# Optimization experiments

Measured on AMD Instinct MI355X. Metric: run time of the kernel, lower is better.

The kernel has to match this reference:

```python
import jax, jax.numpy as jnp
import numpy as np

N_HEAD = 16
ROPE_BASE = 10000.0


def _rope(x, cos, sin):
    # x: [B,H,T,D]; cos/sin: [T,D/2] broadcast over B,H
    half = x.shape[-1] // 2
    x1, x2 = x[..., :half], x[..., half:]
    return jnp.concatenate([x1 * cos - x2 * sin, x1 * sin + x2 * cos], axis=-1)


def setup_inputs() -> dict:
    key = jax.random.key(0)
    k1, k2, k3 = jax.random.split(key, 3)
    C = 2048
    x = jax.random.normal(k1, (4, 2048, C), dtype=jnp.float32)
    w_qkv = jax.random.normal(k2, (C, 3 * C), dtype=jnp.float32) * 0.02
    w_proj = jax.random.normal(k3, (C, C), dtype=jnp.float32) * 0.02
    return {"x": x, "w_qkv": w_qkv, "w_proj": w_proj}


def reference(x, w_qkv, w_proj):
    B, T, C = x.shape
    H = N_HEAD
    D = C // H
    half = D // 2

    qkv = x @ w_qkv  # [B,T,3C]
    q, k, v = jnp.split(qkv, 3, axis=-1)
    # [B,T,C] -> [B,H,T,D]
    q = q.reshape(B, T, H, D).transpose(0, 2, 1, 3)
    k = k.reshape(B, T, H, D).transpose(0, 2, 1, 3)
    v = v.reshape(B, T, H, D).transpose(0, 2, 1, 3)

    # RoPE cache (start_pos = 0, no kv_cache / prefill path)
    inv_freq = 1.0 / (ROPE_BASE ** (jnp.arange(half, dtype=jnp.float32) / half))
    pos = jnp.arange(T, dtype=jnp.float32)
    freqs = pos[:, None] * inv_freq[None, :]  # [T, half]
    cos, sin = jnp.cos(freqs), jnp.sin(freqs)

    q = _rope(q, cos, sin)
    k = _rope(k, cos, sin)

    # scaled dot-product attention with explicit causal mask
    att = jnp.einsum("bhqd,bhkd->bhqk", q, k) / jnp.sqrt(jnp.asarray(D, x.dtype))
    causal = jnp.arange(T)[:, None] >= jnp.arange(T)[None, :]  # [T,T] bool
    att = jnp.where(causal, att, jnp.asarray(-jnp.inf, att.dtype))
    att = jax.nn.softmax(att, axis=-1)
    # dropout = identity (eval mode)
    out = jnp.einsum("bhqk,bhkd->bhqd", att, v)
    out = out.transpose(0, 2, 1, 3).reshape(B, T, C)
    out = out @ w_proj
    return out, k, v  # (output, new kv-cache)
```

## Files before the change

### kernel.cpp

```cpp
#include <hip/hip_runtime.h>
#include <math.h>

#define CDIM 2048
#define TDIM 2048
#define BDIM 4
#define HDIM 16
#define DDIM 128
#define M1   (BDIM * TDIM)
#define N1   (3 * CDIM)
#define KK   CDIM
#define NT   32

typedef unsigned short u16;
typedef __bf16 bf16x8 __attribute__((ext_vector_type(8)));
typedef float f32x4 __attribute__((ext_vector_type(4)));

__device__ __forceinline__ u16 f2b(float f) {
  union { float f; unsigned u; } x; x.f = f;
  unsigned r = x.u + 0x7fffu + ((x.u >> 16) & 1u);
  return (u16)(r >> 16);
}

__device__ __forceinline__ void gload_lds16(const void* g, void* l) {
  __builtin_amdgcn_global_load_lds(
      (__attribute__((address_space(1))) void*)g,
      (__attribute__((address_space(3))) void*)l, 16, 0, 0);
}

__global__ void convert_x(const float* __restrict__ x, u16* __restrict__ xb, int n4) {
  int i = blockIdx.x * blockDim.x + threadIdx.x;
  if (i < n4) {
    float4 v = ((const float4*)x)[i];
    unsigned long long o = (unsigned long long)f2b(v.x)
                         | ((unsigned long long)f2b(v.y) << 16)
                         | ((unsigned long long)f2b(v.z) << 32)
                         | ((unsigned long long)f2b(v.w) << 48);
    ((unsigned long long*)xb)[i] = o;
  }
}

__global__ void transpose_w(const float* __restrict__ w, u16* __restrict__ wt, int K, int N) {
  __shared__ float tile[32][33];
  const int n0 = blockIdx.x * 32, k0 = blockIdx.y * 32;
  const int tx = threadIdx.x & 31, ty = threadIdx.x >> 5;
  for (int r = ty; r < 32; r += 8)
    tile[r][tx] = w[(k0 + r) * N + n0 + tx];
  __syncthreads();
  for (int r = ty; r < 32; r += 8)
    wt[(n0 + r) * K + k0 + tx] = f2b(tile[tx][r]);
}

__global__ void rope_tab(float* __restrict__ cosT, float* __restrict__ sinT) {
  int i = blockIdx.x * blockDim.x + threadIdx.x;
  int t = i >> 6, d = i & 63;
  double inv = pow(10000.0, -(double)d / 64.0);
  double a = (double)t * inv;
  cosT[i] = (float)cos(a);
  sinT[i] = (float)sin(a);
}

__global__ void transpose_v(const float* __restrict__ v, u16* __restrict__ vt) {
  __shared__ float tile[32][33];
  const int bh = blockIdx.z;
  const int t0 = blockIdx.x * 32, d0 = blockIdx.y * 32;
  const int tx = threadIdx.x & 31, ty = threadIdx.x >> 5;
  const float* src = v + (bh * TDIM + t0) * DDIM + d0;
  for (int r = ty; r < 32; r += 8)
    tile[r][tx] = src[r * DDIM + tx];
  __syncthreads();
  u16* dst = vt + (bh * DDIM + d0) * TDIM + t0;
  for (int r = ty; r < 32; r += 8)
    dst[r * TDIM + tx] = f2b(tile[tx][r]);
}


#define VMW4 asm volatile("s_waitcnt vmcnt(4)" ::: "memory");
#define VMW2 asm volatile("s_waitcnt vmcnt(2)" ::: "memory");
#define VMW0 asm volatile("s_waitcnt vmcnt(0)" ::: "memory");
#define NOWAIT

#define GEMM256_TILE(bufA_, bufB_, nA_, nB_, kno_, STG, WMID, WEND)            \
  {                                                                            \
    __builtin_amdgcn_s_barrier();        \
    bf16x8 aX[4][2], aY[4][2], bX[2][2], bY[2][2];                             \
                                                     \
    _Pragma("unroll")                                                          \
    for (int i = 0; i < 4; ++i)                                                \
      _Pragma("unroll")                                                        \
      for (int kh = 0; kh < 2; ++kh)                                           \
        aX[i][kh] = *(const bf16x8*)&(bufA_)[aoff + i * 1024 +                 \
                                             (((kh * 4 + quad) ^ rsw) * 8)];   \
    _Pragma("unroll")                                                          \
    for (int j = 0; j < 2; ++j)                                                \
      _Pragma("unroll")                                                        \
      for (int kh = 0; kh < 2; ++kh)                                           \
        bX[j][kh] = *(const bf16x8*)&(bufB_)[boff + j * 1024 +                 \
                                             (((kh * 4 + quad) ^ rsw) * 8)];   \
                                                          \
    __builtin_amdgcn_s_setprio(1);                                             \
    _Pragma("unroll")                                                          \
    for (int i = 0; i < 4; ++i)                                                \
      _Pragma("unroll")                                                        \
      for (int j = 0; j < 2; ++j)                                              \
        _Pragma("unroll")                                                      \
        for (int kh = 0; kh < 2; ++kh)                                         \
          acc[i][j] = __builtin_amdgcn_mfma_f32_16x16x32_bf16(                 \
              aX[i][kh], bX[j][kh], acc[i][j], 0, 0, 0);                       \
    __builtin_amdgcn_s_setprio(0);                                             \
              \
    _Pragma("unroll")                                                          \
    for (int j = 0; j < 2; ++j)                                                \
      _Pragma("unroll")                                                        \
      for (int kh = 0; kh < 2; ++kh)                                           \
        bY[j][kh] = *(const bf16x8*)&(bufB_)[8192 + boff + j * 1024 +          \
                                             (((kh * 4 + quad) ^ rsw) * 8)];   \
    if (STG) {                                                                 \
      _Pragma("unroll")                                                        \
      for (int q = 0; q < 2; ++q)                                              \
        gload_lds16(AgBase + (q * 128) * KK + (kno_), &(nA_)[q * 4096 + ldsw]);\
      _Pragma("unroll")                                                        \
      for (int q = 0; q < 2; ++q)                                              \
        gload_lds16(BgBase + (q * 128) * KK + (kno_),                          \
                    &(nB_)[q * 4096 + ldsw]);                                  \
    }                                                                          \
    WMID                                                                       \
    __builtin_amdgcn_s_barrier();                       \
                                 \
    __builtin_amdgcn_s_setprio(1);                                             \
    _Pragma("unroll")                                                          \
    for (int i = 0; i < 4; ++i)                                                \
      _Pragma("unroll")                                                        \
      for (int j = 0; j < 2; ++j)                                              \
        _Pragma("unroll")                                                      \
        for (int kh = 0; kh < 2; ++kh)                                         \
          acc[i][2 + j] = __builtin_amdgcn_mfma_f32_16x16x32_bf16(             \
              aX[i][kh], bY[j][kh], acc[i][2 + j], 0, 0, 0);                   \
    __builtin_amdgcn_s_setprio(0);                                             \
             \
    _Pragma("unroll")                                                          \
    for (int i = 0; i < 4; ++i)                                                \
      _Pragma("unroll")                                                        \
      for (int kh = 0; kh < 2; ++kh)                                           \
        aY[i][kh] = *(const bf16x8*)&(bufA_)[8192 + aoff + i * 1024 +          \
                                             (((kh * 4 + quad) ^ rsw) * 8)];   \
    if (STG) {                                                                 \
      _Pragma("unroll")                                                        \
      for (int q = 0; q < 2; ++q)                                              \
        gload_lds16(BgBase + (q * 128 + 32) * KK + (kno_),                     \
                    &(nB_)[8192 + q * 4096 + ldsw]);                           \
    }                                                                          \
                                                          \
    __builtin_amdgcn_s_setprio(1);                                             \
    _Pragma("unroll")                                                          \
    for (int i = 0; i < 4; ++i)                                                \
      _Pragma("unroll")                                                        \
      for (int j = 0; j < 2; ++j)                                              \
        _Pragma("unroll")                                                      \
        for (int kh = 0; kh < 2; ++kh)                                         \
          acc[4 + i][2 + j] = __builtin_amdgcn_mfma_f32_16x16x32_bf16(         \
              aY[i][kh], bY[j][kh], acc[4 + i][2 + j], 0, 0, 0);               \
    __builtin_amdgcn_s_setprio(0);                                             \
    if (STG) {                                                                 \
      _Pragma("unroll")                                                        \
      for (int q = 0; q < 2; ++q)                                              \
        gload_lds16(AgBase + (q * 128 + 64) * KK + (kno_),                     \
                    &(nA_)[8192 + q * 4096 + ldsw]);                           \
    }                                                                          \
                    \
    __builtin_amdgcn_s_setprio(1);                                             \
    _Pragma("unroll")                                                          \
    for (int i = 0; i < 4; ++i)                                                \
      _Pragma("unroll")                                                        \
      for (int j = 0; j < 2; ++j)                                              \
        _Pragma("unroll")                                                      \
        for (int kh = 0; kh < 2; ++kh)                                         \
          acc[4 + i][j] = __builtin_amdgcn_mfma_f32_16x16x32_bf16(             \
              aY[i][kh], bX[j][kh], acc[4 + i][j], 0, 0, 0);                   \
    __builtin_amdgcn_s_setprio(0);                                             \
    WEND                                                                       \
  }

#define GEMM256_MAINLOOP(APTR, BPTR)                                           \
  const int rA = lane >> 3, cA = lane & 7;                                     \
  const int w8r = wave * 8 + rA;                                               \
  const int swz8 = (cA ^ rA) * 8;                                              \
  const u16* AgBase = (APTR) + (m0 + w8r) * KK + swz8;                         \
  const int nb = ((w8r >> 5) * 64) + (w8r & 31);                               \
  const u16* BgBase = (BPTR) + (n0 + nb) * KK + swz8;                          \
  const int ldsw = wave * 512;                                                 \
  const int rsw = c16 & 7;                                                     \
  const int aoff = (((wave >> 2) * 64) + c16) * 64;                            \
  const int boff = (((wave & 3) * 32) + c16) * 64;                             \
  f32x4 acc[8][4];                                                             \
  {                                                                            \
    f32x4 z = {0.f, 0.f, 0.f, 0.f};                                            \
    _Pragma("unroll")                                                          \
    for (int i = 0; i < 8; ++i)                                                \
      _Pragma("unroll")                                                        \
      for (int j = 0; j < 4; ++j) acc[i][j] = z;                               \
  }                                                                            \
     \
  _Pragma("unroll")                                                            \
  for (int q = 0; q < 2; ++q)                                                  \
    gload_lds16(AgBase + (q * 128) * KK, &lds[q * 4096 + ldsw]);               \
  _Pragma("unroll")                                                            \
  for (int q = 0; q < 2; ++q)                                                  \
    gload_lds16(BgBase + (q * 128) * KK, &lds[32768 + q * 4096 + ldsw]);       \
  _Pragma("unroll")                                                            \
  for (int q = 0; q < 2; ++q)                                                  \
    gload_lds16(BgBase + (q * 128 + 32) * KK,                                  \
                &lds[32768 + 8192 + q * 4096 + ldsw]);                         \
  _Pragma("unroll")                                                            \
  for (int q = 0; q < 2; ++q)                                                  \
    gload_lds16(AgBase + (q * 128 + 64) * KK, &lds[8192 + q * 4096 + ldsw]);   \
  VMW2                                                                         \
  for (int kt = 0; kt < NT - 1; ++kt) {                                        \
    const int cur = kt & 1;                                                    \
    const u16* bA = &lds[cur * 16384];                                         \
    const u16* bB = &lds[32768 + cur * 16384];                                 \
    u16* nA = &lds[(cur ^ 1) * 16384];                                         \
    u16* nB = &lds[32768 + (cur ^ 1) * 16384];                                 \
    const int kno = (kt + 1) * 64;                                             \
    GEMM256_TILE(bA, bB, nA, nB, kno, 1, VMW4, VMW2)                           \
  }                                                                            \
           \
  GEMM256_TILE((&lds[16384]), (&lds[32768 + 16384]), (&lds[0]),                \
               (&lds[32768]), 0, 0, VMW0, NOWAIT)

__global__ __launch_bounds__(512, 1) void gemm_qkv(
    const u16* __restrict__ A,
    const u16* __restrict__ Bt,
    const float* __restrict__ cosT, const float* __restrict__ sinT,
    u16* __restrict__ qb, u16* __restrict__ kb,
    float* __restrict__ kout, float* __restrict__ vout)
{
  extern __shared__ __align__(16) u16 lds[];
  const int tid = threadIdx.x, wave = tid >> 6, lane = tid & 63;
  const int quad = lane >> 4, c16 = lane & 15;
  const int bid = blockIdx.y * 24 + blockIdx.x;
  const int swz = (bid & 7) * 96 + (bid >> 3);
  const int m0 = (swz / 24) * 256, n0 = (swz % 24) * 256;

  GEMM256_MAINLOOP(A, Bt)

  float* cbuf = (float*)lds;
  const int mat = n0 >> 11;
  const int hbase = (n0 & 2047) >> 7;
  const float qscale = 0.088388347648318447f;
#pragma unroll
  for (int pass = 0; pass < 4; ++pass) {
    __syncthreads();
    if ((wave >> 2) == (pass >> 1)) {
#pragma unroll
      for (int i = 0; i < 4; ++i) {
        const int mf = (pass & 1) * 4 + i;
#pragma unroll
        for (int j = 0; j < 4; ++j)
#pragma unroll
          for (int r = 0; r < 4; ++r)
            cbuf[(i * 16 + quad * 4 + r) * 260 + (wave & 3) * 64 + j * 16 + c16] = acc[mf][j][r];
      }
    }
    __syncthreads();
#pragma unroll
    for (int it = 0; it < 16; ++it) {
      int p = it * 512 + tid;
      int lr = p >> 7;
      int hc = (p >> 6) & 1;
      int d = p & 63;
      float x1 = cbuf[lr * 260 + hc * 128 + d];
      float x2 = cbuf[lr * 260 + hc * 128 + 64 + d];
      int mg = m0 + pass * 64 + lr;
      int b = mg >> 11, t = mg & 2047;
      int h = hbase + hc;
      int idx = ((b * HDIM + h) * TDIM + t) * DDIM + d;
      if (mat == 2) {
        vout[idx] = x1; vout[idx + 64] = x2;
      } else {
        float cs = cosT[t * 64 + d], sn = sinT[t * 64 + d];
        float o1 = x1 * cs - x2 * sn;
        float o2 = x1 * sn + x2 * cs;
        if (mat == 0) {
          qb[idx] = f2b(o1 * qscale); qb[idx + 64] = f2b(o2 * qscale);
        } else {
          kout[idx] = o1; kout[idx + 64] = o2;
          kb[idx] = f2b(o1); kb[idx + 64] = f2b(o2);
        }
      }
    }
  }
}

__global__ __launch_bounds__(512, 1) void gemm_proj(
    const u16* __restrict__ A,
    const u16* __restrict__ Bt,
    float* __restrict__ out)
{
  extern __shared__ __align__(16) u16 lds[];
  const int tid = threadIdx.x, wave = tid >> 6, lane = tid & 63;
  const int quad = lane >> 4, c16 = lane & 15;
  const int bid = blockIdx.y * 8 + blockIdx.x;
  const int swz = (bid & 7) * 32 + (bid >> 3);
  const int m0 = (swz >> 3) * 256, n0 = (swz & 7) * 256;

  GEMM256_MAINLOOP(A, Bt)

  const int wm = (wave >> 2) * 128, wn = (wave & 3) * 64;
#pragma unroll
  for (int mf = 0; mf < 8; ++mf)
#pragma unroll
    for (int nf = 0; nf < 4; ++nf)
#pragma unroll
      for (int r = 0; r < 4; ++r)
        out[(m0 + wm + mf * 16 + quad * 4 + r) * CDIM + n0 + wn + nf * 16 + c16] =
            acc[mf][nf][r];
}

__global__ __launch_bounds__(256, 2) void attn(
    const u16* __restrict__ qb, const u16* __restrict__ kb,
    const u16* __restrict__ vt, u16* __restrict__ att)
{
  extern __shared__ __align__(16) u16 sh[];
  u16* const psm = sh + 32768;

  const int tid = threadIdx.x, wave = tid >> 6, lane = tid & 63;
  const int quad = lane >> 4, c16 = lane & 15;
  const int bx = blockIdx.x;
  const int bh = blockIdx.y;

  for (int hv = 0; hv < 2; ++hv) {
    const int qt = hv ? (7 - bx) : (bx + 8);
    const int q0 = qt * 128;

    {
      const u16* qg = qb + (bh * TDIM + q0) * DDIM;
      const int rowl = wave * 4 + (lane >> 4);
      const int ch = lane & 15;
#pragma unroll
      for (int r = 0; r < 8; ++r) {
        int row = r * 16 + rowl;
        gload_lds16(qg + row * DDIM + (ch ^ (row & 15)) * 8,
                    &sh[(r * 16 + wave * 4) * 128]);
      }
    }
    __syncthreads();
    bf16x8 qf[2][4];
#pragma unroll
    for (int g = 0; g < 2; ++g)
#pragma unroll
      for (int kp = 0; kp < 4; ++kp)
        qf[g][kp] = *(const bf16x8*)&sh[(g * 64 + wave * 16 + c16) * 128 +
                                        (((kp * 4 + quad) ^ c16) * 8)];
    __syncthreads();

    f32x4 o[2][8];
    f32x4 zero = {0.f, 0.f, 0.f, 0.f};
#pragma unroll
    for (int g = 0; g < 2; ++g)
#pragma unroll
      for (int jd = 0; jd < 8; ++jd) o[g][jd] = zero;
    float mrow[2][4], lrow[2][4];
#pragma unroll
    for (int g = 0; g < 2; ++g)
#pragma unroll
      for (int r = 0; r < 4; ++r) { mrow[g][r] = -INFINITY; lrow[g][r] = 0.f; }

    const int nchunk = 2 * qt + 2;

    const int rowl = wave * 4 + (lane >> 4);
    const int ch = lane & 15;
    const int rowv = wave * 8 + (lane >> 3);
    const int chv = lane & 7;
#define STAGE_KV(kcs, bufbase)                                                 \
    {                                                                          \
      const int kcs0 = (kcs) * 64;                                             \
      const u16* kg = kb + (bh * TDIM + kcs0) * DDIM;                          \
      _Pragma("unroll")                                                        \
      for (int r = 0; r < 4; ++r) {                                            \
        int row = r * 16 + rowl;                                               \
        gload_lds16(kg + row * DDIM + (ch ^ (row & 15)) * 8,                   \
                    &sh[(bufbase) + (r * 16 + wave * 4) * 128]);               \
      }                                                                        \
      const u16* vg = vt + bh * (DDIM * TDIM) + kcs0;                          \
      _Pragma("unroll")                                                        \
      for (int r = 0; r < 4; ++r) {                                            \
        int row = r * 32 + rowv;                                               \
        gload_lds16(vg + row * TDIM + (chv ^ (row & 7)) * 8,                   \
                    &sh[(bufbase) + 8192 + (r * 32 + wave * 8) * 64]);         \
      }                                                                        \
    }

    STAGE_KV(0, 0)

    for (int kc = 0; kc < nchunk; ++kc) {
      const int kc0 = kc * 64;
      const int cur = kc & 1;
      const u16* ksm = sh + cur * 16384;
      const u16* vsm = ksm + 8192;

      if (kc + 1 < nchunk) {
        STAGE_KV(kc + 1, (cur ^ 1) * 16384)
        asm volatile("s_waitcnt vmcnt(8)" ::: "memory");
      } else {
        asm volatile("s_waitcnt vmcnt(0)" ::: "memory");
      }
      asm volatile("s_barrier" ::: "memory");

      f32x4 st[2][4];
#pragma unroll
      for (int g = 0; g < 2; ++g)
#pragma unroll
        for (int j = 0; j < 4; ++j) st[g][j] = zero;
#pragma unroll
      for (int kp = 0; kp < 4; ++kp) {
#pragma unroll
        for (int j = 0; j < 4; ++j) {
          bf16x8 bk = *(const bf16x8*)&ksm[(j * 16 + c16) * 128 +
                                           (((kp * 4 + quad) ^ c16) * 8)];
          st[0][j] = __builtin_amdgcn_mfma_f32_16x16x32_bf16(qf[0][kp], bk, st[0][j], 0, 0, 0);
          st[1][j] = __builtin_amdgcn_mfma_f32_16x16x32_bf16(qf[1][kp], bk, st[1][j], 0, 0, 0);
        }
      }

      u16* const pw = psm + wave * 2048;
      float al2[2][4];
#pragma unroll
      for (int g = 0; g < 2; ++g) {
        const bool dg = (kc >= 2 * qt + g);
        const int qrow_base = q0 + g * 64 + wave * 16 + quad * 4;
#pragma unroll
        for (int r = 0; r < 4; ++r) {
          float mx = -INFINITY;
#pragma unroll
          for (int j = 0; j < 4; ++j) {
            float sv = st[g][j][r];
            if (dg && (kc0 + j * 16 + c16 > qrow_base + r)) sv = -INFINITY;
            st[g][j][r] = sv;
            mx = fmaxf(mx, sv);
          }
          mx = fmaxf(mx, __shfl_xor(mx, 1, 64));
          mx = fmaxf(mx, __shfl_xor(mx, 2, 64));
          mx = fmaxf(mx, __shfl_xor(mx, 4, 64));
          mx = fmaxf(mx, __shfl_xor(mx, 8, 64));
          float mnew = fmaxf(mrow[g][r], mx);
          float al = __expf(mrow[g][r] - mnew);
          mrow[g][r] = mnew;
          al2[g][r] = al;
          float sum = 0.f;
          const int row16 = quad * 4 + r;
#pragma unroll
          for (int j = 0; j < 4; ++j) {
            float p = __expf(st[g][j][r] - mnew);
            sum += p;
            int chunk = (j * 2 + (c16 >> 3)) ^ (row16 & 7);
            pw[g * 1024 + row16 * 64 + chunk * 8 + (c16 & 7)] = f2b(p);
          }
          sum += __shfl_xor(sum, 1, 64);
          sum += __shfl_xor(sum, 2, 64);
          sum += __shfl_xor(sum, 4, 64);
          sum += __shfl_xor(sum, 8, 64);
          lrow[g][r] = lrow[g][r] * al + sum;
        }
#pragma unroll
        for (int jd = 0; jd < 8; ++jd)
#pragma unroll
          for (int r = 0; r < 4; ++r)
            o[g][jd][r] *= al2[g][r];
      }

      asm volatile("s_waitcnt lgkmcnt(0)" ::: "memory");

#pragma unroll
      for (int s = 0; s < 2; ++s) {
        const int chp = ((s * 4 + quad) ^ (c16 & 7)) * 8;
        bf16x8 ap0 = *(const bf16x8*)&pw[c16 * 64 + chp];
        bf16x8 ap1 = *(const bf16x8*)&pw[1024 + c16 * 64 + chp];
#pragma unroll
        for (int jd = 0; jd < 8; ++jd) {
          bf16x8 bv = *(const bf16x8*)&vsm[(jd * 16 + c16) * 64 + chp];
          o[0][jd] = __builtin_amdgcn_mfma_f32_16x16x32_bf16(ap0, bv, o[0][jd], 0, 0, 0);
          o[1][jd] = __builtin_amdgcn_mfma_f32_16x16x32_bf16(ap1, bv, o[1][jd], 0, 0, 0);
        }
      }
      asm volatile("s_barrier" ::: "memory");
    }
#undef STAGE_KV

    const int b = bh >> 4, h = bh & 15;
#pragma unroll
    for (int g = 0; g < 2; ++g) {
      float ri[4];
#pragma unroll
      for (int r = 0; r < 4; ++r) ri[r] = 1.f / lrow[g][r];
#pragma unroll
      for (int jd = 0; jd < 8; ++jd)
#pragma unroll
        for (int r = 0; r < 4; ++r) {
          int t = q0 + g * 64 + wave * 16 + quad * 4 + r;
          att[(b * TDIM + t) * CDIM + h * DDIM + jd * 16 + c16] = f2b(o[g][jd][r] * ri[r]);
        }
    }
    __syncthreads();
  }
}

extern "C" void kernel_launch(void* const* d_in, const int* in_sizes, int n_in,
                              void* d_out, int out_size, void* d_ws, size_t ws_size,
                              hipStream_t stream) {
  (void)in_sizes; (void)n_in; (void)out_size; (void)ws_size;
  const float* x      = (const float*)d_in[0];
  const float* w_qkv  = (const float*)d_in[1];
  const float* w_proj = (const float*)d_in[2];
  float* out  = (float*)d_out;
  float* kout = out + 16777216;
  float* vout = out + 2 * 16777216;

  char* ws = (char*)d_ws;
  u16*   xb     = (u16*)(ws);
  u16*   wqkvT  = (u16*)(ws + 33554432);
  u16*   wprojT = (u16*)(ws + 58720256);
  float* cosT   = (float*)(ws + 67108864);
  float* sinT   = (float*)(ws + 67633152);
  u16*   qb     = (u16*)(ws + 68157440);
  u16*   kb     = (u16*)(ws + 101711872);
  u16*   vt     = (u16*)(ws + 135266304);
  u16*   att    = xb;

  static int attr_set = 0;
  if (!attr_set) {
    hipFuncSetAttribute((const void*)gemm_qkv,
                        hipFuncAttributeMaxDynamicSharedMemorySize, 131072);
    hipFuncSetAttribute((const void*)gemm_proj,
                        hipFuncAttributeMaxDynamicSharedMemorySize, 131072);
    hipFuncSetAttribute((const void*)attn,
                        hipFuncAttributeMaxDynamicSharedMemorySize, 81920);
    attr_set = 1;
  }

  convert_x<<<16384, 256, 0, stream>>>(x, xb, 4194304);
  transpose_w<<<dim3(192, 64), 256, 0, stream>>>(w_qkv, wqkvT, KK, N1);
  transpose_w<<<dim3(64, 64), 256, 0, stream>>>(w_proj, wprojT, KK, CDIM);
  rope_tab<<<512, 256, 0, stream>>>(cosT, sinT);
  gemm_qkv<<<dim3(24, 32), 512, 131072, stream>>>(xb, wqkvT, cosT, sinT, qb, kb, kout, vout);
  transpose_v<<<dim3(64, 4, 64), 256, 0, stream>>>(vout, vt);
  attn<<<dim3(8, 64), 256, 81920, stream>>>(qb, kb, vt, att);
  gemm_proj<<<dim3(8, 32), 512, 131072, stream>>>(att, wprojT, out);
}
```

Measured before the change: 763.1 us.

## Fuse V transpose into QKV epilogue, lazy softmax rescale, exp2 domain, fast rope table

The QKV GEMM epilogue now also writes the transposed bf16 V directly, removing the separate transpose_v kernel and its extra read of V. Attention switches to exp2 by folding log2(e) into the Q scale. It also skips the running-max update and output rescale unless some row's max grows by more than 8. The rope table is computed in float instead of double, and the LDS staging stride is padded from 260 to 261 to reduce bank conflicts. These changes trade a small accuracy risk (float rope, deferred rescaling) for less launch, memory and ALU work.

```diff
diff --git a/kernel.cpp b/kernel.cpp
--- a/kernel.cpp
+++ b/kernel.cpp
@@ -53,24 +53,10 @@
 __global__ void rope_tab(float* __restrict__ cosT, float* __restrict__ sinT) {
   int i = blockIdx.x * blockDim.x + threadIdx.x;
   int t = i >> 6, d = i & 63;
-  double inv = pow(10000.0, -(double)d / 64.0);
-  double a = (double)t * inv;
-  cosT[i] = (float)cos(a);
-  sinT[i] = (float)sin(a);
-}
-
-__global__ void transpose_v(const float* __restrict__ v, u16* __restrict__ vt) {
-  __shared__ float tile[32][33];
-  const int bh = blockIdx.z;
-  const int t0 = blockIdx.x * 32, d0 = blockIdx.y * 32;
-  const int tx = threadIdx.x & 31, ty = threadIdx.x >> 5;
-  const float* src = v + (bh * TDIM + t0) * DDIM + d0;
-  for (int r = ty; r < 32; r += 8)
-    tile[r][tx] = src[r * DDIM + tx];
-  __syncthreads();
-  u16* dst = vt + (bh * DDIM + d0) * TDIM + t0;
-  for (int r = ty; r < 32; r += 8)
-    dst[r * TDIM + tx] = f2b(tile[tx][r]);
+  float inv = exp2f(-(float)d * (13.287712379549449f / 64.0f));
+  float a = (float)t * inv;
+  cosT[i] = cosf(a);
+  sinT[i] = sinf(a);
 }
 
 
@@ -232,7 +218,8 @@
     const u16* __restrict__ Bt,
     const float* __restrict__ cosT, const float* __restrict__ sinT,
     u16* __restrict__ qb, u16* __restrict__ kb,
-    float* __restrict__ kout, float* __restrict__ vout)
+    float* __restrict__ kout, float* __restrict__ vout,
+    u16* __restrict__ vtout)
 {
   extern __shared__ __align__(16) u16 lds[];
   const int tid = threadIdx.x, wave = tid >> 6, lane = tid & 63;
@@ -246,7 +233,7 @@
   float* cbuf = (float*)lds;
   const int mat = n0 >> 11;
   const int hbase = (n0 & 2047) >> 7;
-  const float qscale = 0.088388347648318447f;
+  const float qscale = 0.1275178689414753f;
 #pragma unroll
   for (int pass = 0; pass < 4; ++pass) {
     __syncthreads();
@@ -258,7 +245,7 @@
         for (int j = 0; j < 4; ++j)
 #pragma unroll
           for (int r = 0; r < 4; ++r)
-            cbuf[(i * 16 + quad * 4 + r) * 260 + (wave & 3) * 64 + j * 16 + c16] = acc[mf][j][r];
+            cbuf[(i * 16 + quad * 4 + r) * 261 + (wave & 3) * 64 + j * 16 + c16] = acc[mf][j][r];
       }
     }
     __syncthreads();
@@ -268,8 +255,8 @@
       int lr = p >> 7;
       int hc = (p >> 6) & 1;
       int d = p & 63;
-      float x1 = cbuf[lr * 260 + hc * 128 + d];
-      float x2 = cbuf[lr * 260 + hc * 128 + 64 + d];
+      float x1 = cbuf[lr * 261 + hc * 128 + d];
+      float x2 = cbuf[lr * 261 + hc * 128 + 64 + d];
       int mg = m0 + pass * 64 + lr;
       int b = mg >> 11, t = mg & 2047;
       int h = hbase + hc;
@@ -288,6 +275,20 @@
         }
       }
     }
+    if (mat == 2) {
+#pragma unroll
+      for (int it = 0; it < 16; ++it) {
+        int p = it * 512 + tid;
+        int tl = p & 63;
+        int c2 = p >> 6;
+        float xA = cbuf[tl * 261 + c2];
+        float xB = cbuf[tl * 261 + 128 + c2];
+        int mg = m0 + pass * 64 + tl;
+        int b = mg >> 11, t = mg & 2047;
+        vtout[((b * HDIM + hbase) * DDIM + c2) * TDIM + t] = f2b(xA);
+        vtout[((b * HDIM + hbase + 1) * DDIM + c2) * TDIM + t] = f2b(xB);
+      }
+    }
   }
 }
 
@@ -428,6 +429,8 @@
       for (int g = 0; g < 2; ++g) {
         const bool dg = (kc >= 2 * qt + g);
         const int qrow_base = q0 + g * 64 + wave * 16 + quad * 4;
+        float mxr[4];
+        bool needb = false;
 #pragma unroll
         for (int r = 0; r < 4; ++r) {
           float mx = -INFINITY;
@@ -442,15 +445,27 @@
           mx = fmaxf(mx, __shfl_xor(mx, 2, 64));
           mx = fmaxf(mx, __shfl_xor(mx, 4, 64));
           mx = fmaxf(mx, __shfl_xor(mx, 8, 64));
-          float mnew = fmaxf(mrow[g][r], mx);
-          float al = __expf(mrow[g][r] - mnew);
-          mrow[g][r] = mnew;
+          mxr[r] = mx;
+          needb |= (mx > mrow[g][r] + 8.0f);
+        }
+        const bool need = __any(needb);
+#pragma unroll
+        for (int r = 0; r < 4; ++r) {
+          float mnew, al;
+          if (need) {
+            mnew = fmaxf(mrow[g][r], mxr[r]);
+            al = exp2f(mrow[g][r] - mnew);
+            mrow[g][r] = mnew;
+          } else {
+            mnew = mrow[g][r];
+            al = 1.0f;
+          }
           al2[g][r] = al;
           float sum = 0.f;
           const int row16 = quad * 4 + r;
 #pragma unroll
           for (int j = 0; j < 4; ++j) {
-            float p = __expf(st[g][j][r] - mnew);
+            float p = exp2f(st[g][j][r] - mnew);
             sum += p;
             int chunk = (j * 2 + (c16 >> 3)) ^ (row16 & 7);
             pw[g * 1024 + row16 * 64 + chunk * 8 + (c16 & 7)] = f2b(p);
@@ -461,11 +476,13 @@
           sum += __shfl_xor(sum, 8, 64);
           lrow[g][r] = lrow[g][r] * al + sum;
         }
-#pragma unroll
-        for (int jd = 0; jd < 8; ++jd)
-#pragma unroll
-          for (int r = 0; r < 4; ++r)
-            o[g][jd][r] *= al2[g][r];
+        if (need) {
+#pragma unroll
+          for (int jd = 0; jd < 8; ++jd)
+#pragma unroll
+            for (int r = 0; r < 4; ++r)
+              o[g][jd][r] *= al2[g][r];
+        }
       }
 
       asm volatile("s_waitcnt lgkmcnt(0)" ::: "memory");
@@ -541,8 +558,7 @@
   transpose_w<<<dim3(192, 64), 256, 0, stream>>>(w_qkv, wqkvT, KK, N1);
   transpose_w<<<dim3(64, 64), 256, 0, stream>>>(w_proj, wprojT, KK, CDIM);
   rope_tab<<<512, 256, 0, stream>>>(cosT, sinT);
-  gemm_qkv<<<dim3(24, 32), 512, 131072, stream>>>(xb, wqkvT, cosT, sinT, qb, kb, kout, vout);
-  transpose_v<<<dim3(64, 4, 64), 256, 0, stream>>>(vout, vt);
+  gemm_qkv<<<dim3(24, 32), 512, 131072, stream>>>(xb, wqkvT, cosT, sinT, qb, kb, kout, vout, vt);
   attn<<<dim3(8, 64), 256, 81920, stream>>>(qb, kb, vt, att);
   gemm_proj<<<dim3(8, 32), 512, 131072, stream>>>(att, wprojT, out);
 }
```

Measured after the change: 773.4 us. About the same (+1.4%).
